# Kernel optimization log

Hardware: AMD Instinct MI355X
Metric: run time of the kernel (lower is better)

## Reference

```python
import jax, jax.numpy as jnp
import numpy as np

H = 8          # num_head
HD = 64        # head_dim = hidden_dim // num_head
WIN = 33       # atten_window_size (odd)
MIN_SCORE = -1e9


def setup_inputs() -> dict:
    key = jax.random.key(0)
    ks = jax.random.split(key, 12)
    B, S, D = 8, 4096, 512
    scale = 1.0 / np.sqrt(D).astype(np.float32)

    def lin_w(k):
        return jax.random.normal(k, (D, D), jnp.float32) * scale

    return {
        "query": jax.random.normal(ks[0], (B, S, D), jnp.float32),
        "key": jax.random.normal(ks[1], (B, S, D), jnp.float32),
        "value": jax.random.normal(ks[2], (B, S, D), jnp.float32),
        "mask": jax.random.randint(ks[3], (B, S), 0, 2).astype(bool),
        "Wq": lin_w(ks[4]), "bq": jax.random.normal(ks[5], (D,), jnp.float32) * 0.02,
        "Wk": lin_w(ks[6]), "bk": jax.random.normal(ks[7], (D,), jnp.float32) * 0.02,
        "Wv": lin_w(ks[8]), "bv": jax.random.normal(ks[9], (D,), jnp.float32) * 0.02,
        "Wo": lin_w(ks[10]), "bo": jax.random.normal(ks[11], (D,), jnp.float32) * 0.02,
    }


def reference(query, key, value, mask, Wq, bq, Wk, bk, Wv, bv, Wo, bo):
    B, S, D = query.shape
    half = min(WIN // 2, S // 2)

    def proj_split(x, W, b):
        # nn.Linear: x @ W.T + b; then split heads and flatten (B,H) -> B*H
        y = x @ W.T + b
        return y.reshape(B, S, H, HD).transpose(0, 2, 1, 3).reshape(B * H, S, HD)

    q = proj_split(query, Wq, bq)   # [BH, S, HD]
    k = proj_split(key, Wk, bk)
    v = proj_split(value, Wv, bv)
    # mask expanded over heads; True = masked (LocalAttention semantics)
    m = jnp.broadcast_to(mask[:, None, :], (B, H, S)).reshape(B * H, S)

    # banded scores: one [BH, S] vector per window offset (no sqrt(head_dim) scaling,
    # faithful to LocalAttention)
    scores = []
    for off in range(-half, half + 1):
        if off < 0:
            w = jnp.sum(q[:, -off:] * k[:, :off], axis=-1)
            w = jnp.where(m[:, :off], MIN_SCORE, w)
            w = jnp.pad(w, ((0, 0), (-off, 0)), constant_values=MIN_SCORE)
        elif off == 0:
            w = jnp.where(m, MIN_SCORE, jnp.sum(q * k, axis=-1))
        else:
            w = jnp.sum(q[:, :-off] * k[:, off:], axis=-1)
            w = jnp.where(m[:, off:], MIN_SCORE, w)
            w = jnp.pad(w, ((0, 0), (0, off)), constant_values=MIN_SCORE)
        scores.append(w)
    probs = jax.nn.softmax(jnp.stack(scores, axis=-1), axis=-1)  # [BH, S, 2*half+1]

    # weighted gather of values along the band (dropout=0 -> identity)
    out = jnp.zeros_like(v)
    for i, off in enumerate(range(-half, half + 1)):
        p = probs[:, :, i:i + 1]
        if off < 0:
            out = out + jnp.pad(p[:, -off:] * v[:, :off], ((0, 0), (-off, 0), (0, 0)))
        elif off == 0:
            out = out + p * v
        else:
            out = out + jnp.pad(p[:, :-off] * v[:, off:], ((0, 0), (0, off), (0, 0)))

    out = out.reshape(B, H, S, HD).transpose(0, 2, 1, 3).reshape(B, S, D)
    return out @ Wo.T + bo
```

## Files before the change

### kernel.cpp

```cpp
#include <hip/hip_runtime.h>
#include <hip/hip_bf16.h>
#include <stdint.h>

#define BB 8
#define SS 4096
#define DD 512
#define HH 8
#define HDIM 64

typedef unsigned short u16;
typedef __attribute__((ext_vector_type(4))) float f32x4;
typedef __attribute__((ext_vector_type(4))) short s16x4;
typedef __attribute__((ext_vector_type(8))) short s16x8;
typedef __attribute__((ext_vector_type(4))) unsigned int u32x4;

__device__ __forceinline__ u16 f2bf(float f) {
  uint32_t x = __builtin_bit_cast(uint32_t, f);
  x += 0x7fffu + ((x >> 16) & 1u);
  return (u16)(x >> 16);
}
__device__ __forceinline__ float bf2f(u16 u) {
  uint32_t x = (uint32_t)u << 16;
  return __builtin_bit_cast(float, x);
}
__device__ __forceinline__ uint32_t cvtpk(float a, float b) {
  uint32_t d;
  asm("v_cvt_pk_bf16_f32 %0, %1, %2" : "=v"(d) : "v"(a), "v"(b));
  return d;
}

__device__ __forceinline__ void gld_lds16(const void* g, void* l) {
  __builtin_amdgcn_global_load_lds((const __attribute__((address_space(1))) void*)g,
                                   (__attribute__((address_space(3))) void*)l, 16, 0, 0);
}

__global__ void cvt_weights(const float* __restrict__ w0, const float* __restrict__ w1,
                            const float* __restrict__ w2, const float* __restrict__ w3,
                            u16* __restrict__ out) {
  int i = blockIdx.x * blockDim.x + threadIdx.x;
  const int n = DD * DD;
  if (i < n) {
    out[i]         = f2bf(w0[i]);
    out[n + i]     = f2bf(w1[i]);
    out[2 * n + i] = f2bf(w2[i]);
    out[3 * n + i] = f2bf(w3[i]);
  }
}

__global__ void mask_unpack(const void* __restrict__ mraw, uint8_t* __restrict__ mk, int n) {
  __shared__ int bad[3];
  __shared__ int mode;
  const int t = threadIdx.x;
  if (t < 3) bad[t] = 0;
  __syncthreads();
  const uint32_t* w = (const uint32_t*)mraw;
  const uint32_t x = w[t];
  const bool w01 = (x == 0u) || (x == 1u);
  const uint32_t ob = x | (x >> 8) | (x >> 16) | (x >> 24);
  const bool u01 = ((ob & 0xFEu) == 0u);
  if (!w01) atomicAdd(&bad[0], 1);
  if (!u01) atomicAdd(&bad[1], 1);
  __syncthreads();
  if (t == 0) mode = (bad[0] == 0) ? 0 : (bad[1] == 0 ? 1 : 2);
  __syncthreads();
  const int md = mode;
  for (int i = blockIdx.x * 256 + t; i < n; i += gridDim.x * 256) {
    uint8_t v;
    if (md == 0)      v = (uint8_t)(w[i] & 1u);
    else if (md == 1) v = ((const uint8_t*)mraw)[i] ? 1 : 0;
    else              v = (w[i] != 0u) ? 1 : 0;
    mk[i] = v;
  }
}

template <typename TA, typename TC>
__global__ __launch_bounds__(256, 2)
void gemm97(const TA* __restrict__ A, const u16* __restrict__ Bw,
            const float* __restrict__ bias, TC* __restrict__ C,
            int M, int N, int K) {
  constexpr bool AF32 = (sizeof(TA) == 4);
  constexpr int ABYTES = AF32 ? 128 * 64 * 4 : 128 * 64 * 2;
  __shared__ __align__(16) char sA[ABYTES];
  __shared__ __align__(16) u16 sB[128 * 64];

  const int tid = threadIdx.x;
  const int lane = tid & 63, wv = tid >> 6;
  const int wr = (wv >> 1) * 64, wc = (wv & 1) * 64;
  const int c = lane & 15, g = lane >> 4;
  const int lid = blockIdx.x;
  const int rb = (lid >> 5) * 8 + (lid & 7);
  const int cb = (lid >> 3) & 3;
  const int col0 = cb * 128, row0 = rb * 128;

  const int srB = tid >> 3, cBc = (tid & 7) ^ ((tid >> 3) & 7);
  const u16* b_src = Bw + (size_t)(col0 + srB) * K + cBc * 8;
  const int srA = tid >> 4, cAc = (tid & 15) ^ (tid >> 4);
  const TA* a_srcF = A + (size_t)(row0 + srA) * K + cAc * 4;
  const TA* a_srcH = A + (size_t)(row0 + srB) * K + cBc * 8;

  f32x4 acc[4][4];
#pragma unroll
  for (int a = 0; a < 4; ++a)
#pragma unroll
    for (int b = 0; b < 4; ++b) acc[a][b] = (f32x4){0.f, 0.f, 0.f, 0.f};

  const int nkt = K / 64;
  for (int kt = 0; kt < nkt; ++kt) {
    __syncthreads();
    const int ko = kt * 64;
    if constexpr (AF32) {
#pragma unroll
      for (int i = 0; i < 8; ++i)
        gld_lds16(a_srcF + (size_t)i * 16 * K + ko, sA + i * 4096 + wv * 1024);
    } else {
#pragma unroll
      for (int i = 0; i < 4; ++i)
        gld_lds16(a_srcH + (size_t)i * 32 * K + ko, sA + i * 4096 + wv * 1024);
    }
#pragma unroll
    for (int i = 0; i < 4; ++i)
      gld_lds16(b_src + (size_t)i * 32 * K + ko, (char*)sB + i * 4096 + wv * 1024);
    __syncthreads();

#pragma unroll
    for (int ks = 0; ks < 2; ++ks) {
      s16x8 af[4], bq[4];
#pragma unroll
      for (int mf = 0; mf < 4; ++mf) {
        const int row = wr + mf * 16 + c;
        if constexpr (AF32) {
          const int bc = ks * 128 + g * 32;
          const f32x4 lo4 = *(const f32x4*)(sA + row * 256 + ((bc) ^ (c << 4)));
          const f32x4 hi4 = *(const f32x4*)(sA + row * 256 + ((bc + 16) ^ (c << 4)));
          const u32x4 dd = (u32x4){cvtpk(lo4[0], lo4[1]), cvtpk(lo4[2], lo4[3]),
                                   cvtpk(hi4[0], hi4[1]), cvtpk(hi4[2], hi4[3])};
          af[mf] = __builtin_bit_cast(s16x8, dd);
        } else {
          const int bc = ks * 64 + g * 16;
          af[mf] = *(const s16x8*)(sA + row * 128 + (bc ^ ((c & 7) << 4)));
        }
      }
#pragma unroll
      for (int nf = 0; nf < 4; ++nf) {
        const int row = wc + nf * 16 + c;
        const int bc = ks * 64 + g * 16;
        bq[nf] = *(const s16x8*)((char*)sB + row * 128 + (bc ^ ((c & 7) << 4)));
      }
#pragma unroll
      for (int mf = 0; mf < 4; ++mf)
#pragma unroll
        for (int nf = 0; nf < 4; ++nf)
          acc[mf][nf] = __builtin_amdgcn_mfma_f32_16x16x32_bf16(af[mf], bq[nf], acc[mf][nf], 0, 0, 0);
    }
  }

#pragma unroll
  for (int nf = 0; nf < 4; ++nf) {
    const int col = col0 + wc + nf * 16 + c;
    const float bv = bias[col];
#pragma unroll
    for (int mf = 0; mf < 4; ++mf) {
#pragma unroll
      for (int i = 0; i < 4; ++i) {
        const int row = row0 + wr + mf * 16 + g * 4 + i;
        const float v = acc[mf][nf][i] + bv;
        if constexpr (sizeof(TC) == 4) C[(size_t)row * N + col] = v;
        else                           C[(size_t)row * N + col] = (TC)f2bf(v);
      }
    }
  }
}

__device__ __forceinline__ void hilo8(const f32x4& a0, const f32x4& a1, s16x8& h, s16x8& l) {
#pragma unroll
  for (int j = 0; j < 4; ++j) {
    const float f = a0[j];
    const u16 hb = f2bf(f);
    h[j] = (short)hb;
    l[j] = (short)f2bf(f - bf2f(hb));
  }
#pragma unroll
  for (int j = 0; j < 4; ++j) {
    const float f = a1[j];
    const u16 hb = f2bf(f);
    h[4 + j] = (short)hb;
    l[4 + j] = (short)f2bf(f - bf2f(hb));
  }
}

__global__ __launch_bounds__(256, 4)
void attn_mfma(const float* __restrict__ Qp, const float* __restrict__ Kp,
               const u16* __restrict__ Vp, const uint8_t* __restrict__ mk,
               u16* __restrict__ O) {
  __shared__ u16 sKh[96 * 72];
  __shared__ u16 sKl[96 * 68];
  __shared__ u16 sVT[64 * 104];
  __shared__ u16 sM[96];

  const int bh = blockIdx.x;
  const int b = bh >> 3, h = bh & 7;
  const int s0 = blockIdx.y * 64;
  const int tid = threadIdx.x;

  const int wv = tid >> 6, lane = tid & 63;
  const int c = lane & 15, g = lane >> 4;
  const int qloc = wv * 16 + c;
  const int qrow = s0 + qloc;

  const float* qp = Qp + ((size_t)(b * SS + qrow)) * DD + h * HDIM;
  f32x4 qa0[2], qa1[2];
#pragma unroll
  for (int ks = 0; ks < 2; ++ks) {
    qa0[ks] = *(const f32x4*)(qp + 32 * ks + 4 * g);
    qa1[ks] = *(const f32x4*)(qp + 32 * ks + 16 + 4 * g);
  }

#pragma unroll
  for (int it = 0; it < 3; ++it) {
    const int item = tid + it * 256;
    const int row = item >> 3, j = item & 7;
    const int ks = j >> 2, g2 = j & 3;
    const int gr = s0 - 16 + row;
    f32x4 a0 = (f32x4){0.f, 0.f, 0.f, 0.f}, a1 = (f32x4){0.f, 0.f, 0.f, 0.f};
    if (gr >= 0 && gr < SS) {
      const float* kp = Kp + ((size_t)(b * SS + gr)) * DD + h * HDIM + ks * 32 + g2 * 4;
      a0 = *(const f32x4*)kp;
      a1 = *(const f32x4*)(kp + 16);
    }
    s16x8 hh, ll;
    hilo8(a0, a1, hh, ll);
    *(s16x8*)&sKh[row * 72 + j * 8] = hh;
    *(s16x4*)&sKl[row * 68 + j * 8]     = (s16x4){ll[0], ll[1], ll[2], ll[3]};
    *(s16x4*)&sKl[row * 68 + j * 8 + 4] = (s16x4){ll[4], ll[5], ll[6], ll[7]};
  }
#pragma unroll
  for (int it = 0; it < 3; ++it) {
    const int item = tid + it * 256;
    const int k = item >> 3, dg8 = item & 7;
    const int gr = s0 - 16 + k;
    s16x8 vv = (s16x8){0, 0, 0, 0, 0, 0, 0, 0};
    if (gr >= 0 && gr < SS)
      vv = *(const s16x8*)(Vp + ((size_t)(b * SS + gr)) * DD + h * HDIM + dg8 * 8);
    const int ks = k >> 5, rem = k & 31, hf = rem >> 4, q = rem & 15;
    const int g2 = q >> 2, i2 = q & 3;
    const int pos = (ks * 4 + g2) * 8 + hf * 4 + i2;
#pragma unroll
    for (int i = 0; i < 8; ++i) sVT[(dg8 * 8 + i) * 104 + pos] = (u16)vv[i];
  }
  for (int r = tid; r < 96; r += 256) {
    const int gr = s0 - 16 + r;
    sM[r] = (gr < 0 || gr >= SS || mk[b * SS + gr]) ? 1 : 0;
  }
  __syncthreads();

  s16x8 qh[2], qlo[2];
#pragma unroll
  for (int ks = 0; ks < 2; ++ks) hilo8(qa0[ks], qa1[ks], qh[ks], qlo[ks]);

  f32x4 st[6];
#pragma unroll
  for (int kt = 0; kt < 6; ++kt) st[kt] = (f32x4){0.f, 0.f, 0.f, 0.f};
#pragma unroll
  for (int kt = 0; kt < 6; ++kt) {
    const int rb72 = (kt * 16 + c) * 72;
    const int rb68 = (kt * 16 + c) * 68;
#pragma unroll
    for (int ks = 0; ks < 2; ++ks) {
      const s16x8 kh = *(const s16x8*)&sKh[rb72 + ks * 32 + g * 8];
      const s16x4 l0 = *(const s16x4*)&sKl[rb68 + ks * 32 + g * 8];
      const s16x4 l1 = *(const s16x4*)&sKl[rb68 + ks * 32 + g * 8 + 4];
      const s16x8 kl = (s16x8){l0[0], l0[1], l0[2], l0[3], l1[0], l1[1], l1[2], l1[3]};
      st[kt] = __builtin_amdgcn_mfma_f32_16x16x32_bf16(kh, qh[ks], st[kt], 0, 0, 0);
      st[kt] = __builtin_amdgcn_mfma_f32_16x16x32_bf16(kh, qlo[ks], st[kt], 0, 0, 0);
      st[kt] = __builtin_amdgcn_mfma_f32_16x16x32_bf16(kl, qh[ks], st[kt], 0, 0, 0);
    }
  }

  float mx = -3.0e9f;
#pragma unroll
  for (int kt = 0; kt < 6; ++kt) {
#pragma unroll
    for (int i = 0; i < 4; ++i) {
      const int kl_ = kt * 16 + 4 * g + i;
      const int delta = kl_ - 16 - qloc;
      float v;
      if (delta < -16 || delta > 16) v = -2.0e9f;
      else if (sM[kl_])              v = -1.0e9f;
      else                           v = st[kt][i];
      st[kt][i] = v;
      mx = fmaxf(mx, v);
    }
  }
  mx = fmaxf(mx, __shfl_xor(mx, 16));
  mx = fmaxf(mx, __shfl_xor(mx, 32));
  float sum = 0.f;
#pragma unroll
  for (int kt = 0; kt < 6; ++kt) {
#pragma unroll
    for (int i = 0; i < 4; ++i) {
      const float e = __expf(st[kt][i] - mx);
      st[kt][i] = e;
      sum += e;
    }
  }
  sum += __shfl_xor(sum, 16);
  sum += __shfl_xor(sum, 32);
  const float inv = 1.f / sum;

  s16x8 ph[3];
#pragma unroll
  for (int ks = 0; ks < 3; ++ks) {
#pragma unroll
    for (int i = 0; i < 4; ++i) {
      ph[ks][i]     = (short)f2bf(st[2 * ks][i]);
      ph[ks][4 + i] = (short)f2bf(st[2 * ks + 1][i]);
    }
  }

  f32x4 ot[4];
#pragma unroll
  for (int dt = 0; dt < 4; ++dt) ot[dt] = (f32x4){0.f, 0.f, 0.f, 0.f};
#pragma unroll
  for (int dt = 0; dt < 4; ++dt) {
    const int rbv = (dt * 16 + c) * 104;
#pragma unroll
    for (int ks = 0; ks < 3; ++ks) {
      const s16x8 vh = *(const s16x8*)&sVT[rbv + ks * 32 + g * 8];
      ot[dt] = __builtin_amdgcn_mfma_f32_16x16x32_bf16(vh, ph[ks], ot[dt], 0, 0, 0);
    }
  }

  u16* op = O + ((size_t)(b * SS + qrow)) * DD + h * HDIM;
#pragma unroll
  for (int dt = 0; dt < 4; ++dt) {
    s16x4 pk;
#pragma unroll
    for (int i = 0; i < 4; ++i) pk[i] = (short)f2bf(ot[dt][i] * inv);
    *(s16x4*)&op[dt * 16 + 4 * g] = pk;
  }
}

__global__ __launch_bounds__(256)
void attn_win(const u16* __restrict__ Qp, const u16* __restrict__ Kp,
              const u16* __restrict__ Vp, const uint8_t* __restrict__ mk,
              u16* __restrict__ O) {
  constexpr int KR = 96;
  __shared__ float sK[KR][HDIM];
  __shared__ float sV[KR][HDIM];
  __shared__ float sMf[KR];

  const int bh = blockIdx.x;
  const int b = bh >> 3, h = bh & 7;
  const int s0 = blockIdx.y * 64;
  const int tid = threadIdx.x;

  for (int c = tid; c < KR * 16; c += 256) {
    const int row = c >> 4, c4 = c & 15;
    const int gr = s0 - 16 + row;
    float kv[4], vv[4];
    if (gr >= 0 && gr < SS) {
      const size_t base = ((size_t)(b * SS + gr)) * DD + h * HDIM + c4 * 4;
      const s16x4 kk = *(const s16x4*)(Kp + base);
      const s16x4 vx = *(const s16x4*)(Vp + base);
#pragma unroll
      for (int i = 0; i < 4; ++i) { kv[i] = bf2f((u16)kk[i]); vv[i] = bf2f((u16)vx[i]); }
    } else {
#pragma unroll
      for (int i = 0; i < 4; ++i) { kv[i] = 0.f; vv[i] = 0.f; }
    }
#pragma unroll
    for (int i = 0; i < 4; ++i) {
      const int d = c4 * 4 + i;
      const int pd = (d & 15) * 4 + (d >> 4);
      sK[row][pd] = kv[i];
      sV[row][pd] = vv[i];
    }
  }
  for (int r = tid; r < KR; r += 256) {
    const int gr = s0 - 16 + r;
    sMf[r] = (gr < 0 || gr >= SS || mk[b * SS + gr]) ? 1.f : 0.f;
  }
  __syncthreads();

  const int wv = tid >> 6, lane = tid & 63;
  const int g = lane >> 4, d16 = lane & 15;

  for (int rr = 0; rr < 16; rr += 4) {
    const int lr = wv * 16 + rr + g;
    const int srow = s0 + lr;
    const u16* qp = Qp + ((size_t)(b * SS + srow)) * DD + h * HDIM;
    float q0 = bf2f(qp[d16]), q1 = bf2f(qp[d16 + 16]), q2 = bf2f(qp[d16 + 32]), q3 = bf2f(qp[d16 + 48]);
    float sc[33];
#pragma unroll
    for (int o = 0; o < 33; ++o) {
      const f32x4 kk = *(const f32x4*)&sK[lr + o][d16 * 4];
      float p = q0 * kk[0] + q1 * kk[1] + q2 * kk[2] + q3 * kk[3];
      p += __shfl_xor(p, 1);
      p += __shfl_xor(p, 2);
      p += __shfl_xor(p, 4);
      p += __shfl_xor(p, 8);
      sc[o] = (sMf[lr + o] != 0.f) ? -1.0e9f : p;
    }
    float mx = sc[0];
#pragma unroll
    for (int o = 1; o < 33; ++o) mx = fmaxf(mx, sc[o]);
    float sum = 0.f;
#pragma unroll
    for (int o = 0; o < 33; ++o) { const float e = __expf(sc[o] - mx); sc[o] = e; sum += e; }
    const float inv = 1.f / sum;
    f32x4 acc = (f32x4){0.f, 0.f, 0.f, 0.f};
#pragma unroll
    for (int o = 0; o < 33; ++o) {
      const f32x4 vx = *(const f32x4*)&sV[lr + o][d16 * 4];
      acc += (sc[o] * inv) * vx;
    }
    u16* op = O + ((size_t)(b * SS + srow)) * DD + h * HDIM;
    op[d16]      = f2bf(acc[0]);
    op[d16 + 16] = f2bf(acc[1]);
    op[d16 + 32] = f2bf(acc[2]);
    op[d16 + 48] = f2bf(acc[3]);
  }
}

extern "C" void kernel_launch(void* const* d_in, const int* in_sizes, int n_in,
                              void* d_out, int out_size, void* d_ws, size_t ws_size,
                              hipStream_t stream) {
  const float* query = (const float*)d_in[0];
  const float* key   = (const float*)d_in[1];
  const float* value = (const float*)d_in[2];
  const void*  mraw  = d_in[3];
  const float* Wq = (const float*)d_in[4];
  const float* bq = (const float*)d_in[5];
  const float* Wk = (const float*)d_in[6];
  const float* bk = (const float*)d_in[7];
  const float* Wv = (const float*)d_in[8];
  const float* bv = (const float*)d_in[9];
  const float* Wo = (const float*)d_in[10];
  const float* bo = (const float*)d_in[11];

  const int M = BB * SS, N = DD, K = DD;

  char* ws = (char*)d_ws;
  size_t off = 0;
  auto carve = [&](size_t bytes) -> char* {
    char* p = ws + off;
    off = (off + bytes + 255) & ~(size_t)255;
    return p;
  };
  u16* wAll   = (u16*)carve((size_t)4 * DD * DD * sizeof(u16));
  uint8_t* mk = (uint8_t*)carve((size_t)BB * SS);

  const size_t qk_f32 = (size_t)M * DD * 4;
  const size_t v_b16  = (size_t)M * DD * 2;
  const bool f32p = (off + 2 * qk_f32 + 2 * v_b16 + 1024) <= ws_size;

  cvt_weights<<<(DD * DD + 255) / 256, 256, 0, stream>>>(Wq, Wk, Wv, Wo, wAll);
  mask_unpack<<<16, 256, 0, stream>>>(mraw, mk, BB * SS);

  const dim3 gg((M / 128) * (N / 128));
  const dim3 ga(BB * HH, SS / 64);

  if (f32p) {
    float* Qf = (float*)carve(qk_f32);
    float* Kf = (float*)carve(qk_f32);
    u16*   Vb = (u16*)carve(v_b16);
    u16*   AO = (u16*)carve(v_b16);
    gemm97<float, float><<<gg, 256, 0, stream>>>(query, wAll,               bq, Qf, M, N, K);
    gemm97<float, float><<<gg, 256, 0, stream>>>(key,   wAll + DD * DD,     bk, Kf, M, N, K);
    gemm97<float, u16><<<gg, 256, 0, stream>>>(value, wAll + 2 * DD * DD, bv, Vb, M, N, K);
    attn_mfma<<<ga, 256, 0, stream>>>(Qf, Kf, Vb, mk, AO);
    gemm97<u16, float><<<gg, 256, 0, stream>>>(AO, wAll + 3 * DD * DD, bo, (float*)d_out, M, N, K);
  } else {
    u16* Qb = (u16*)carve(v_b16);
    u16* Kb = (u16*)carve(v_b16);
    u16* Vb = (u16*)carve(v_b16);
    u16* AO = (u16*)carve(v_b16);
    gemm97<float, u16><<<gg, 256, 0, stream>>>(query, wAll,               bq, Qb, M, N, K);
    gemm97<float, u16><<<gg, 256, 0, stream>>>(key,   wAll + DD * DD,     bk, Kb, M, N, K);
    gemm97<float, u16><<<gg, 256, 0, stream>>>(value, wAll + 2 * DD * DD, bv, Vb, M, N, K);
    attn_win<<<ga, 256, 0, stream>>>(Qb, Kb, Vb, mk, AO);
    gemm97<u16, float><<<gg, 256, 0, stream>>>(AO, wAll + 3 * DD * DD, bo, (float*)d_out, M, N, K);
  }
}
```

Measured before the change: 234.1 us.

## Process four query tiles per attention block with register-prefetched next tile

Each attn_mfma block now walks four consecutive 64-row query tiles. Global loads for the next tile's K, V, mask and Q are issued into registers before the current tile's MFMA and softmax work, then written to shared memory after a barrier. This hides global load latency behind compute and cuts the grid by 4x, but it adds register pressure under launch_bounds(256,4), two extra barriers per tile, and fewer blocks to spread across CUs.

```diff
diff --git a/kernel.cpp b/kernel.cpp
--- a/kernel.cpp
+++ b/kernel.cpp
@@ -188,6 +188,8 @@
   }
 }
 
+#define ACH 4
+
 __global__ __launch_bounds__(256, 4)
 void attn_mfma(const float* __restrict__ Qp, const float* __restrict__ Kp,
                const u16* __restrict__ Vp, const uint8_t* __restrict__ mk,
@@ -199,144 +201,180 @@
 
   const int bh = blockIdx.x;
   const int b = bh >> 3, h = bh & 7;
-  const int s0 = blockIdx.y * 64;
+  const int base0 = blockIdx.y * (64 * ACH);
   const int tid = threadIdx.x;
 
   const int wv = tid >> 6, lane = tid & 63;
   const int c = lane & 15, g = lane >> 4;
   const int qloc = wv * 16 + c;
-  const int qrow = s0 + qloc;
-
-  const float* qp = Qp + ((size_t)(b * SS + qrow)) * DD + h * HDIM;
-  f32x4 qa0[2], qa1[2];
-#pragma unroll
-  for (int ks = 0; ks < 2; ++ks) {
-    qa0[ks] = *(const f32x4*)(qp + 32 * ks + 4 * g);
-    qa1[ks] = *(const f32x4*)(qp + 32 * ks + 16 + 4 * g);
-  }
-
-#pragma unroll
-  for (int it = 0; it < 3; ++it) {
-    const int item = tid + it * 256;
-    const int row = item >> 3, j = item & 7;
-    const int ks = j >> 2, g2 = j & 3;
-    const int gr = s0 - 16 + row;
-    f32x4 a0 = (f32x4){0.f, 0.f, 0.f, 0.f}, a1 = (f32x4){0.f, 0.f, 0.f, 0.f};
-    if (gr >= 0 && gr < SS) {
-      const float* kp = Kp + ((size_t)(b * SS + gr)) * DD + h * HDIM + ks * 32 + g2 * 4;
-      a0 = *(const f32x4*)kp;
-      a1 = *(const f32x4*)(kp + 16);
-    }
-    s16x8 hh, ll;
-    hilo8(a0, a1, hh, ll);
-    *(s16x8*)&sKh[row * 72 + j * 8] = hh;
-    *(s16x4*)&sKl[row * 68 + j * 8]     = (s16x4){ll[0], ll[1], ll[2], ll[3]};
-    *(s16x4*)&sKl[row * 68 + j * 8 + 4] = (s16x4){ll[4], ll[5], ll[6], ll[7]};
-  }
-#pragma unroll
-  for (int it = 0; it < 3; ++it) {
-    const int item = tid + it * 256;
-    const int k = item >> 3, dg8 = item & 7;
-    const int gr = s0 - 16 + k;
-    s16x8 vv = (s16x8){0, 0, 0, 0, 0, 0, 0, 0};
-    if (gr >= 0 && gr < SS)
-      vv = *(const s16x8*)(Vp + ((size_t)(b * SS + gr)) * DD + h * HDIM + dg8 * 8);
-    const int ks = k >> 5, rem = k & 31, hf = rem >> 4, q = rem & 15;
-    const int g2 = q >> 2, i2 = q & 3;
-    const int pos = (ks * 4 + g2) * 8 + hf * 4 + i2;
-#pragma unroll
-    for (int i = 0; i < 8; ++i) sVT[(dg8 * 8 + i) * 104 + pos] = (u16)vv[i];
-  }
-  for (int r = tid; r < 96; r += 256) {
-    const int gr = s0 - 16 + r;
-    sM[r] = (gr < 0 || gr >= SS || mk[b * SS + gr]) ? 1 : 0;
-  }
+
+  const int krow0 = tid >> 3, kj = tid & 7;
+  const int kks = kj >> 2, kg2 = kj & 3;
+  const int vk0 = tid >> 3, vdg8 = tid & 7;
+
+  f32x4 kA0[3], kA1[3];
+  s16x8 vR[3];
+  u16 mR = 1;
+  f32x4 qn0[2], qn1[2];
+
+  auto issue_loads = [&](int cs) {
+#pragma unroll
+    for (int it = 0; it < 3; ++it) {
+      const int row = krow0 + it * 32;
+      const int gr = cs - 16 + row;
+      if (gr >= 0 && gr < SS) {
+        const float* kp = Kp + ((size_t)(b * SS + gr)) * DD + h * HDIM + kks * 32 + kg2 * 4;
+        kA0[it] = *(const f32x4*)kp;
+        kA1[it] = *(const f32x4*)(kp + 16);
+      } else {
+        kA0[it] = (f32x4){0.f, 0.f, 0.f, 0.f};
+        kA1[it] = (f32x4){0.f, 0.f, 0.f, 0.f};
+      }
+    }
+#pragma unroll
+    for (int it = 0; it < 3; ++it) {
+      const int k = vk0 + it * 32;
+      const int gr = cs - 16 + k;
+      if (gr >= 0 && gr < SS)
+        vR[it] = *(const s16x8*)(Vp + ((size_t)(b * SS + gr)) * DD + h * HDIM + vdg8 * 8);
+      else
+        vR[it] = (s16x8){0, 0, 0, 0, 0, 0, 0, 0};
+    }
+    if (tid < 96) {
+      const int gr = cs - 16 + tid;
+      mR = (gr < 0 || gr >= SS || mk[b * SS + gr]) ? 1 : 0;
+    }
+    const float* qp = Qp + ((size_t)(b * SS + cs + qloc)) * DD + h * HDIM;
+#pragma unroll
+    for (int ks = 0; ks < 2; ++ks) {
+      qn0[ks] = *(const f32x4*)(qp + 32 * ks + 4 * g);
+      qn1[ks] = *(const f32x4*)(qp + 32 * ks + 16 + 4 * g);
+    }
+  };
+
+  auto write_stage = [&]() {
+#pragma unroll
+    for (int it = 0; it < 3; ++it) {
+      const int row = krow0 + it * 32;
+      s16x8 hh, ll;
+      hilo8(kA0[it], kA1[it], hh, ll);
+      *(s16x8*)&sKh[row * 72 + kj * 8] = hh;
+      *(s16x4*)&sKl[row * 68 + kj * 8]     = (s16x4){ll[0], ll[1], ll[2], ll[3]};
+      *(s16x4*)&sKl[row * 68 + kj * 8 + 4] = (s16x4){ll[4], ll[5], ll[6], ll[7]};
+    }
+#pragma unroll
+    for (int it = 0; it < 3; ++it) {
+      const int k = vk0 + it * 32;
+      const int ks = k >> 5, rem = k & 31, hf = rem >> 4, q = rem & 15;
+      const int g2 = q >> 2, i2 = q & 3;
+      const int pos = (ks * 4 + g2) * 8 + hf * 4 + i2;
+#pragma unroll
+      for (int i = 0; i < 8; ++i) sVT[(vdg8 * 8 + i) * 104 + pos] = (u16)vR[it][i];
+    }
+    if (tid < 96) sM[tid] = mR;
+  };
+
+  issue_loads(base0);
+  write_stage();
   __syncthreads();
 
-  s16x8 qh[2], qlo[2];
-#pragma unroll
-  for (int ks = 0; ks < 2; ++ks) hilo8(qa0[ks], qa1[ks], qh[ks], qlo[ks]);
-
-  f32x4 st[6];
-#pragma unroll
-  for (int kt = 0; kt < 6; ++kt) st[kt] = (f32x4){0.f, 0.f, 0.f, 0.f};
-#pragma unroll
-  for (int kt = 0; kt < 6; ++kt) {
-    const int rb72 = (kt * 16 + c) * 72;
-    const int rb68 = (kt * 16 + c) * 68;
-#pragma unroll
-    for (int ks = 0; ks < 2; ++ks) {
-      const s16x8 kh = *(const s16x8*)&sKh[rb72 + ks * 32 + g * 8];
-      const s16x4 l0 = *(const s16x4*)&sKl[rb68 + ks * 32 + g * 8];
-      const s16x4 l1 = *(const s16x4*)&sKl[rb68 + ks * 32 + g * 8 + 4];
-      const s16x8 kl = (s16x8){l0[0], l0[1], l0[2], l0[3], l1[0], l1[1], l1[2], l1[3]};
-      st[kt] = __builtin_amdgcn_mfma_f32_16x16x32_bf16(kh, qh[ks], st[kt], 0, 0, 0);
-      st[kt] = __builtin_amdgcn_mfma_f32_16x16x32_bf16(kh, qlo[ks], st[kt], 0, 0, 0);
-      st[kt] = __builtin_amdgcn_mfma_f32_16x16x32_bf16(kl, qh[ks], st[kt], 0, 0, 0);
-    }
-  }
-
-  float mx = -3.0e9f;
-#pragma unroll
-  for (int kt = 0; kt < 6; ++kt) {
-#pragma unroll
-    for (int i = 0; i < 4; ++i) {
-      const int kl_ = kt * 16 + 4 * g + i;
-      const int delta = kl_ - 16 - qloc;
-      float v;
-      if (delta < -16 || delta > 16) v = -2.0e9f;
-      else if (sM[kl_])              v = -1.0e9f;
-      else                           v = st[kt][i];
-      st[kt][i] = v;
-      mx = fmaxf(mx, v);
-    }
-  }
-  mx = fmaxf(mx, __shfl_xor(mx, 16));
-  mx = fmaxf(mx, __shfl_xor(mx, 32));
-  float sum = 0.f;
-#pragma unroll
-  for (int kt = 0; kt < 6; ++kt) {
-#pragma unroll
-    for (int i = 0; i < 4; ++i) {
-      const float e = __expf(st[kt][i] - mx);
-      st[kt][i] = e;
-      sum += e;
-    }
-  }
-  sum += __shfl_xor(sum, 16);
-  sum += __shfl_xor(sum, 32);
-  const float inv = 1.f / sum;
-
-  s16x8 ph[3];
-#pragma unroll
-  for (int ks = 0; ks < 3; ++ks) {
-#pragma unroll
-    for (int i = 0; i < 4; ++i) {
-      ph[ks][i]     = (short)f2bf(st[2 * ks][i]);
-      ph[ks][4 + i] = (short)f2bf(st[2 * ks + 1][i]);
-    }
-  }
-
-  f32x4 ot[4];
-#pragma unroll
-  for (int dt = 0; dt < 4; ++dt) ot[dt] = (f32x4){0.f, 0.f, 0.f, 0.f};
-#pragma unroll
-  for (int dt = 0; dt < 4; ++dt) {
-    const int rbv = (dt * 16 + c) * 104;
+  for (int t = 0; t < ACH; ++t) {
+    const int s0 = base0 + t * 64;
+    const int qrow = s0 + qloc;
+
+    s16x8 qh[2], qlo[2];
+#pragma unroll
+    for (int ks = 0; ks < 2; ++ks) hilo8(qn0[ks], qn1[ks], qh[ks], qlo[ks]);
+
+    if (t + 1 < ACH) issue_loads(base0 + (t + 1) * 64);
+
+    f32x4 st[6];
+#pragma unroll
+    for (int kt = 0; kt < 6; ++kt) st[kt] = (f32x4){0.f, 0.f, 0.f, 0.f};
+#pragma unroll
+    for (int kt = 0; kt < 6; ++kt) {
+      const int rb72 = (kt * 16 + c) * 72;
+      const int rb68 = (kt * 16 + c) * 68;
+#pragma unroll
+      for (int ks = 0; ks < 2; ++ks) {
+        const s16x8 kh = *(const s16x8*)&sKh[rb72 + ks * 32 + g * 8];
+        const s16x4 l0 = *(const s16x4*)&sKl[rb68 + ks * 32 + g * 8];
+        const s16x4 l1 = *(const s16x4*)&sKl[rb68 + ks * 32 + g * 8 + 4];
+        const s16x8 kl = (s16x8){l0[0], l0[1], l0[2], l0[3], l1[0], l1[1], l1[2], l1[3]};
+        st[kt] = __builtin_amdgcn_mfma_f32_16x16x32_bf16(kh, qh[ks], st[kt], 0, 0, 0);
+        st[kt] = __builtin_amdgcn_mfma_f32_16x16x32_bf16(kh, qlo[ks], st[kt], 0, 0, 0);
+        st[kt] = __builtin_amdgcn_mfma_f32_16x16x32_bf16(kl, qh[ks], st[kt], 0, 0, 0);
+      }
+    }
+
+    float mx = -3.0e9f;
+#pragma unroll
+    for (int kt = 0; kt < 6; ++kt) {
+#pragma unroll
+      for (int i = 0; i < 4; ++i) {
+        const int kl_ = kt * 16 + 4 * g + i;
+        const int delta = kl_ - 16 - qloc;
+        float v;
+        if (delta < -16 || delta > 16) v = -2.0e9f;
+        else if (sM[kl_])              v = -1.0e9f;
+        else                           v = st[kt][i];
+        st[kt][i] = v;
+        mx = fmaxf(mx, v);
+      }
+    }
+    mx = fmaxf(mx, __shfl_xor(mx, 16));
+    mx = fmaxf(mx, __shfl_xor(mx, 32));
+    float sum = 0.f;
+#pragma unroll
+    for (int kt = 0; kt < 6; ++kt) {
+#pragma unroll
+      for (int i = 0; i < 4; ++i) {
+        const float e = __expf(st[kt][i] - mx);
+        st[kt][i] = e;
+        sum += e;
+      }
+    }
+    sum += __shfl_xor(sum, 16);
+    sum += __shfl_xor(sum, 32);
+    const float inv = 1.f / sum;
+
+    s16x8 ph[3];
 #pragma unroll
     for (int ks = 0; ks < 3; ++ks) {
-      const s16x8 vh = *(const s16x8*)&sVT[rbv + ks * 32 + g * 8];
-      ot[dt] = __builtin_amdgcn_mfma_f32_16x16x32_bf16(vh, ph[ks], ot[dt], 0, 0, 0);
-    }
-  }
-
-  u16* op = O + ((size_t)(b * SS + qrow)) * DD + h * HDIM;
-#pragma unroll
-  for (int dt = 0; dt < 4; ++dt) {
-    s16x4 pk;
-#pragma unroll
-    for (int i = 0; i < 4; ++i) pk[i] = (short)f2bf(ot[dt][i] * inv);
-    *(s16x4*)&op[dt * 16 + 4 * g] = pk;
+#pragma unroll
+      for (int i = 0; i < 4; ++i) {
+        ph[ks][i]     = (short)f2bf(st[2 * ks][i]);
+        ph[ks][4 + i] = (short)f2bf(st[2 * ks + 1][i]);
+      }
+    }
+
+    f32x4 ot[4];
+#pragma unroll
+    for (int dt = 0; dt < 4; ++dt) ot[dt] = (f32x4){0.f, 0.f, 0.f, 0.f};
+#pragma unroll
+    for (int dt = 0; dt < 4; ++dt) {
+      const int rbv = (dt * 16 + c) * 104;
+#pragma unroll
+      for (int ks = 0; ks < 3; ++ks) {
+        const s16x8 vh = *(const s16x8*)&sVT[rbv + ks * 32 + g * 8];
+        ot[dt] = __builtin_amdgcn_mfma_f32_16x16x32_bf16(vh, ph[ks], ot[dt], 0, 0, 0);
+      }
+    }
+
+    u16* op = O + ((size_t)(b * SS + qrow)) * DD + h * HDIM;
+#pragma unroll
+    for (int dt = 0; dt < 4; ++dt) {
+      s16x4 pk;
+#pragma unroll
+      for (int i = 0; i < 4; ++i) pk[i] = (short)f2bf(ot[dt][i] * inv);
+      *(s16x4*)&op[dt * 16 + 4 * g] = pk;
+    }
+
+    __syncthreads();
+    if (t + 1 < ACH) {
+      write_stage();
+      __syncthreads();
+    }
   }
 }
 
@@ -458,7 +496,7 @@
   mask_unpack<<<16, 256, 0, stream>>>(mraw, mk, BB * SS);
 
   const dim3 gg((M / 128) * (N / 128));
-  const dim3 ga(BB * HH, SS / 64);
+  const dim3 ga(BB * HH, SS / (64 * ACH));
 
   if (f32p) {
     float* Qf = (float*)carve(qk_f32);
@@ -471,6 +509,7 @@
     attn_mfma<<<ga, 256, 0, stream>>>(Qf, Kf, Vb, mk, AO);
     gemm97<u16, float><<<gg, 256, 0, stream>>>(AO, wAll + 3 * DD * DD, bo, (float*)d_out, M, N, K);
   } else {
+    const dim3 ga1(BB * HH, SS / 64);
     u16* Qb = (u16*)carve(v_b16);
     u16* Kb = (u16*)carve(v_b16);
     u16* Vb = (u16*)carve(v_b16);
@@ -478,7 +517,7 @@
     gemm97<float, u16><<<gg, 256, 0, stream>>>(query, wAll,               bq, Qb, M, N, K);
     gemm97<float, u16><<<gg, 256, 0, stream>>>(key,   wAll + DD * DD,     bk, Kb, M, N, K);
     gemm97<float, u16><<<gg, 256, 0, stream>>>(value, wAll + 2 * DD * DD, bv, Vb, M, N, K);
-    attn_win<<<ga, 256, 0, stream>>>(Qb, Kb, Vb, mk, AO);
+    attn_win<<<ga1, 256, 0, stream>>>(Qb, Kb, Vb, mk, AO);
     gemm97<u16, float><<<gg, 256, 0, stream>>>(AO, wAll + 3 * DD * DD, bo, (float*)d_out, M, N, K);
   }
 }
```

Result: faster. 228.5 us (-2.4%).
